# Kernel tuning notes

Measured on AMD Instinct MI355X. Metric: run time of the kernel, lower is better.

The kernel has to match this reference:

```python
import jax, jax.numpy as jnp
import numpy as np

N, D, K = 131072, 64, 512
COMMITMENT_COST = 0.25
DECAY = 0.99
EPSILON = 1e-05


def setup_inputs() -> dict:
    key = jax.random.key(0)
    k1, k2, k3 = jax.random.split(key, 3)
    return {
        "inputs": jax.random.normal(k1, (N, D), dtype=jnp.float32),
        "embedding_weight": jax.random.normal(k2, (K, D), dtype=jnp.float32),
        "ema_w": jax.random.normal(k3, (K, D), dtype=jnp.float32),
        "ema_cluster_size": jnp.zeros((K,), dtype=jnp.float32),
    }


def reference(inputs, embedding_weight, ema_w, ema_cluster_size):
    num_embeddings = embedding_weight.shape[0]
    distances = (
        jnp.sum(inputs ** 2, axis=1, keepdims=True)
        + jnp.sum(embedding_weight ** 2, axis=1)
        - 2.0 * jnp.matmul(inputs, embedding_weight.T)
    )
    encoding_indices = jnp.argmin(distances, axis=1)  # [N]
    # dense one-hot (returned by the module); float32 instead of torch double
    encodings = jax.nn.one_hot(encoding_indices, num_embeddings, dtype=jnp.float32)
    # encodings @ W is just a codebook gather
    quantized = jnp.take(embedding_weight, encoding_indices, axis=0)  # [N, D]

    # ---- EMA codebook update (training path; all detached from autodiff) ----
    counts = jax.ops.segment_sum(
        jnp.ones((inputs.shape[0],), dtype=jnp.float32),
        encoding_indices, num_segments=num_embeddings)  # == encodings.sum(0)
    new_cluster_size = ema_cluster_size * DECAY + (1.0 - DECAY) * counts
    n = jnp.sum(new_cluster_size)
    new_cluster_size = (new_cluster_size + EPSILON) / (n + num_embeddings * EPSILON) * n
    # dw = encodings^T @ inputs -> scatter-add of inputs per code
    dw = jax.ops.segment_sum(inputs, encoding_indices, num_segments=num_embeddings)
    new_ema_w = ema_w * DECAY + (1.0 - DECAY) * dw
    new_embedding = new_ema_w / new_cluster_size[:, None]
    new_cluster_size = jax.lax.stop_gradient(new_cluster_size)
    new_ema_w = jax.lax.stop_gradient(new_ema_w)
    new_embedding = jax.lax.stop_gradient(new_embedding)

    # commitment loss (quantized detached)
    e_latent_loss = jnp.mean((jax.lax.stop_gradient(quantized) - inputs) ** 2)
    loss = COMMITMENT_COST * e_latent_loss
    # straight-through estimator
    quantized_st = inputs + jax.lax.stop_gradient(quantized - inputs)

    avg_probs = jnp.mean(encodings, axis=0)
    perplexity = jnp.exp(-jnp.sum(avg_probs * jnp.log(avg_probs + 1e-10)))
    return (loss, quantized_st, perplexity, encodings,
            new_embedding, new_cluster_size, new_ema_w)
```

## Files before the change

### kernel.cpp

```cpp
#include <hip/hip_runtime.h>

#define NROWS 131072
#define DDIM  64
#define KCODE 512

#define QUANT_OFF 1LL
#define PERP_OFF  8388609LL
#define ENC_OFF   8388610LL
#define EMB_OFF   75497474LL
#define CS_OFF    75530242LL
#define EMAW_OFF  75530754LL

#define WS_COUNTS 0
#define WS_NEGWN  512
#define WS_SSE    1024
#define WS_DW     1040
#define WS_ZERO_FLOATS 33808
#define WS_OFF    33808
#define WS_POS    34320
#define WS_IDX    34832
#define WS_BUCKET 165904
#define WS_WHI    296976
#define WS_WMID   313360
#define WS_WLO    329744

using short8 = __attribute__((ext_vector_type(8))) short;
using f32x4  = __attribute__((ext_vector_type(4))) float;

#define MFMA(a, b, c) __builtin_amdgcn_mfma_f32_16x16x32_bf16((a), (b), (c), 0, 0, 0)

__device__ inline unsigned short bf16_rne(float x) {
    unsigned u = __float_as_uint(x);
    unsigned r = u + 0x7FFFu + ((u >> 16) & 1u);
    return (unsigned short)(r >> 16);
}
__device__ inline float bf16_to_f(unsigned short h) {
    return __uint_as_float((unsigned)h << 16);
}
__device__ inline void split3(const float* v, short8& h8, short8& m8, short8& l8) {
#pragma unroll
    for (int j = 0; j < 8; ++j) {
        float x = v[j];
        unsigned short h = bf16_rne(x);
        float m_ = x - bf16_to_f(h);
        unsigned short m = bf16_rne(m_);
        float l_ = m_ - bf16_to_f(m);
        unsigned short l = bf16_rne(l_);
        h8[j] = (short)h; m8[j] = (short)m; l8[j] = (short)l;
    }
}

__global__ __launch_bounds__(256) void prep_kernel(
    const float* __restrict__ W, ushort* __restrict__ whi,
    ushort* __restrict__ wmid, ushort* __restrict__ wlo,
    float* __restrict__ negwn, float* __restrict__ enc) {
    if (blockIdx.x == 8) {
        if (threadIdx.x == 0) {
            enc[0] = 0.f; enc[1] = 0.f;
            enc[67108862ULL] = 0.f; enc[67108863ULL] = 0.f;
        }
        for (int k = threadIdx.x; k < KCODE; k += 256) {
            const float4* wr = reinterpret_cast<const float4*>(&W[(size_t)k * DDIM]);
            float s = 0.f;
#pragma unroll
            for (int i = 0; i < DDIM / 4; ++i) {
                float4 v = wr[i];
                s += v.x * v.x + v.y * v.y + v.z * v.z + v.w * v.w;
            }
            negwn[k] = -0.5f * s;
        }
        return;
    }
    int t = blockIdx.x * 256 + threadIdx.x;
    int lane = t & 63;
    int code = (t >> 6) * 16 + (lane & 15);
    int kbase = (lane >> 4) * 8;
    int obase = t * 16;
#pragma unroll
    for (int kh = 0; kh < 2; ++kh) {
        float xbuf[8];
#pragma unroll
        for (int j = 0; j < 8; ++j) xbuf[j] = W[code * 64 + kh * 32 + kbase + j];
        short8 h8, m8, l8;
        split3(xbuf, h8, m8, l8);
#pragma unroll
        for (int j = 0; j < 8; ++j) {
            whi[obase + kh * 8 + j]  = (ushort)h8[j];
            wmid[obase + kh * 8 + j] = (ushort)m8[j];
            wlo[obase + kh * 8 + j]  = (ushort)l8[j];
        }
    }
}

__global__ __launch_bounds__(256) void vq_main_kernel(
    const float* __restrict__ X, const ushort* __restrict__ WHI,
    const ushort* __restrict__ WMID, const ushort* __restrict__ WLO,
    const float* __restrict__ negwn, const float* __restrict__ W,
    float* __restrict__ counts, float* __restrict__ sse_g,
    int* __restrict__ idx_out, float* __restrict__ outq) {

    __shared__ int rowIdx[128];
    const int tid = threadIdx.x;
    const int wave = tid >> 6, lane = tid & 63;
    const int col = lane & 15, kg = lane >> 4;
    const int row0 = blockIdx.x * 128;
    const int rowbase = row0 + wave * 32;

    short8 xh[2][2], xm[2][2], xl[2][2];
#pragma unroll
    for (int t = 0; t < 2; ++t) {
        int row = rowbase + t * 16 + col;
#pragma unroll
        for (int kh = 0; kh < 2; ++kh) {
            const float4* p = reinterpret_cast<const float4*>(&X[row * 64 + kh * 32 + kg * 8]);
            float4 a = p[0], b = p[1];
            float xbuf[8] = {a.x, a.y, a.z, a.w, b.x, b.y, b.z, b.w};
            split3(xbuf, xh[t][kh], xm[t][kh], xl[t][kh]);
        }
    }

    float bestV[2][4]; int bestC[2][4];
#pragma unroll
    for (int t = 0; t < 2; ++t)
#pragma unroll
        for (int i = 0; i < 4; ++i) { bestV[t][i] = -3.4e38f; bestC[t][i] = 0; }

    for (int c = 0; c < 32; ++c) {
        const short8* ph = reinterpret_cast<const short8*>(&WHI[(c * 64 + lane) * 16]);
        const short8* pm = reinterpret_cast<const short8*>(&WMID[(c * 64 + lane) * 16]);
        const short8* pl = reinterpret_cast<const short8*>(&WLO[(c * 64 + lane) * 16]);
        short8 wh0 = ph[0], wh1 = ph[1];
        short8 wm0 = pm[0], wm1 = pm[1];
        short8 wl0 = pl[0], wl1 = pl[1];
        float wn = negwn[c * 16 + col];
#pragma unroll
        for (int t = 0; t < 2; ++t) {
            f32x4 acc = {0.f, 0.f, 0.f, 0.f};
            acc = MFMA(xh[t][0], wl0, acc); acc = MFMA(xh[t][1], wl1, acc);
            acc = MFMA(xl[t][0], wh0, acc); acc = MFMA(xl[t][1], wh1, acc);
            acc = MFMA(xm[t][0], wm0, acc); acc = MFMA(xm[t][1], wm1, acc);
            acc = MFMA(xh[t][0], wm0, acc); acc = MFMA(xh[t][1], wm1, acc);
            acc = MFMA(xm[t][0], wh0, acc); acc = MFMA(xm[t][1], wh1, acc);
            acc = MFMA(xh[t][0], wh0, acc); acc = MFMA(xh[t][1], wh1, acc);
#pragma unroll
            for (int i = 0; i < 4; ++i) {
                float r = acc[i] + wn;
                if (r > bestV[t][i]) { bestV[t][i] = r; bestC[t][i] = c; }
            }
        }
    }

#pragma unroll
    for (int t = 0; t < 2; ++t)
#pragma unroll
        for (int i = 0; i < 4; ++i) {
            float v = bestV[t][i];
            int ix = bestC[t][i] * 16 + col;
#pragma unroll
            for (int m = 1; m <= 8; m <<= 1) {
                float ov = __shfl_xor(v, m);
                int   oi = __shfl_xor(ix, m);
                if (ov > v || (ov == v && oi < ix)) { v = ov; ix = oi; }
            }
            if (col == 0) rowIdx[wave * 32 + t * 16 + kg * 4 + i] = ix;
        }
    __syncthreads();

    float ssel = 0.f;
    for (int u = tid; u < 128 * 16; u += 256) {
        int r = u >> 4, d4 = (u & 15) << 2;
        int ix = rowIdx[r];
        float4 wv = *reinterpret_cast<const float4*>(&W[ix * 64 + d4]);
        float4 xv = *reinterpret_cast<const float4*>(&X[(size_t)(row0 + r) * 64 + d4]);
        float dx = wv.x - xv.x, dy = wv.y - xv.y, dz = wv.z - xv.z, dw4 = wv.w - xv.w;
        ssel += dx * dx + dy * dy + dz * dz + dw4 * dw4;
        size_t ob = (size_t)(row0 + r) * 64 + d4;
        outq[ob + 0] = xv.x + dx;
        outq[ob + 1] = xv.y + dy;
        outq[ob + 2] = xv.z + dz;
        outq[ob + 3] = xv.w + dw4;
    }
#pragma unroll
    for (int m = 32; m >= 1; m >>= 1) ssel += __shfl_xor(ssel, m);
    if (lane == 0) atomicAdd(sse_g, ssel);

    if (tid < 128) {
        int ix = rowIdx[tid];
        idx_out[row0 + tid] = ix;
        atomicAdd(&counts[ix], 1.0f);
    }
}

__global__ void enc_ones_kernel(const int* __restrict__ idx, float* __restrict__ enc) {
    int i = blockIdx.x * 256 + threadIdx.x;
    enc[(size_t)i * KCODE + idx[i]] = 1.0f;
}

__global__ void prefix_kernel(const float* __restrict__ counts,
                              int* __restrict__ off, int* __restrict__ pos) {
    __shared__ int tmp[512];
    int t = threadIdx.x;
    int c = (int)counts[t];
    tmp[t] = c;
    __syncthreads();
    int val = c;
    for (int s = 1; s < 512; s <<= 1) {
        int add = (t >= s) ? tmp[t - s] : 0;
        __syncthreads();
        val += add; tmp[t] = val;
        __syncthreads();
    }
    int excl = val - c;
    off[t] = excl; pos[t] = excl;
}

__global__ void scatter_kernel(const int* __restrict__ idx, int* __restrict__ pos,
                               int* __restrict__ bucket) {
    int i = blockIdx.x * 256 + threadIdx.x;
    int k = idx[i];
    int p = atomicAdd(&pos[k], 1);
    bucket[p] = (k << 17) | i;
}

__global__ __launch_bounds__(256) void dwsum_kernel(
    const float* __restrict__ X, const int* __restrict__ bucket,
    float* __restrict__ dw) {
    const int lane = threadIdx.x & 63;
    const int gwave = (blockIdx.x * 256 + threadIdx.x) >> 6;
    const int r0 = gwave * 16;
    int v = bucket[r0];
    int k = v >> 17, row = v & 0x1FFFF;
    float acc = 0.f;
#pragma unroll
    for (int i = 0; i < 16; ++i) {
        acc += X[(size_t)row * 64 + lane];
        if (i + 1 < 16) {
            int nv = bucket[r0 + i + 1];
            int nk = nv >> 17, nrow = nv & 0x1FFFF;
            if (nk != k) {
                atomicAdd(&dw[k * 64 + lane], acc);
                acc = 0.f; k = nk;
            }
            row = nrow;
        }
    }
    atomicAdd(&dw[k * 64 + lane], acc);
}

__global__ __launch_bounds__(512) void finalize_kernel(
    const float* __restrict__ ema_w, const float* __restrict__ ema_cs,
    const float* __restrict__ counts, const float* __restrict__ dw,
    const float* __restrict__ sse_g, float* __restrict__ out) {

    __shared__ float red[512];
    __shared__ float cs_sh[512];
    int t = threadIdx.x;

    float cnt = counts[t];
    float raw = ema_cs[t] * 0.99f + 0.01f * cnt;
    red[t] = raw;
    __syncthreads();
    for (int s = 256; s > 0; s >>= 1) {
        if (t < s) red[t] += red[t + s];
        __syncthreads();
    }
    float n = red[0];
    __syncthreads();

    float ncs = (raw + 1e-5f) / (n + (float)KCODE * 1e-5f) * n;
    out[CS_OFF + t] = ncs;
    cs_sh[t] = ncs;

    float avg = cnt / (float)NROWS;
    red[t] = avg * logf(avg + 1e-10f);
    __syncthreads();
    for (int s = 256; s > 0; s >>= 1) {
        if (t < s) red[t] += red[t + s];
        __syncthreads();
    }
    if (t == 0) {
        out[PERP_OFF] = expf(-red[0]);
        out[0] = 0.25f * sse_g[0] / ((float)NROWS * (float)DDIM);
    }
    __syncthreads();

    for (int i = t; i < KCODE * DDIM; i += 512) {
        float ne = ema_w[i] * 0.99f + 0.01f * dw[i];
        out[EMAW_OFF + i] = ne;
        out[EMB_OFF + i] = ne / cs_sh[i >> 6];
    }
}

extern "C" void kernel_launch(void* const* d_in, const int* in_sizes, int n_in,
                              void* d_out, int out_size, void* d_ws, size_t ws_size,
                              hipStream_t stream) {
    const float* X      = (const float*)d_in[0];
    const float* W      = (const float*)d_in[1];
    const float* ema_w  = (const float*)d_in[2];
    const float* ema_cs = (const float*)d_in[3];
    float* out = (float*)d_out;
    float* ws  = (float*)d_ws;

    float*  counts = ws + WS_COUNTS;
    float*  negwn  = ws + WS_NEGWN;
    float*  sse    = ws + WS_SSE;
    float*  dw     = ws + WS_DW;
    int*    off    = (int*)(ws + WS_OFF);
    int*    pos    = (int*)(ws + WS_POS);
    int*    idx    = (int*)(ws + WS_IDX);
    int*    bucket = (int*)(ws + WS_BUCKET);
    ushort* whi    = (ushort*)(ws + WS_WHI);
    ushort* wmid   = (ushort*)(ws + WS_WMID);
    ushort* wlo    = (ushort*)(ws + WS_WLO);

    float* enc = out + ENC_OFF;

    (void)hipMemsetAsync(d_ws, 0, (size_t)WS_ZERO_FLOATS * sizeof(float), stream);
    (void)hipMemsetAsync(enc + 2, 0, 268435440ULL, stream);

    prep_kernel<<<9, 256, 0, stream>>>(W, whi, wmid, wlo, negwn, enc);
    vq_main_kernel<<<NROWS / 128, 256, 0, stream>>>(X, whi, wmid, wlo, negwn, W,
                                                    counts, sse, idx,
                                                    out + QUANT_OFF);
    enc_ones_kernel<<<NROWS / 256, 256, 0, stream>>>(idx, out + ENC_OFF);
    prefix_kernel<<<1, 512, 0, stream>>>(counts, off, pos);
    scatter_kernel<<<NROWS / 256, 256, 0, stream>>>(idx, pos, bucket);
    dwsum_kernel<<<NROWS / 16 / 4, 256, 0, stream>>>(X, bucket, dw);
    finalize_kernel<<<1, 512, 0, stream>>>(ema_w, ema_cs, counts, dw, sse, out);
}
```

Before: 296.0 us.

## Fuse one-hot zeroing and ones writes into the main VQ kernel

The separate memset of the dense one-hot encodings buffer and the enc_ones kernel are removed. Instead, each thread of the main distance/argmin kernel zeroes half of one row of the encodings with nontemporal 8-byte stores, spread across the codebook loop. After the argmin it writes the 1.0 for that row. The aim is to overlap the large zero-fill with MFMA compute and to drop a kernel launch plus an index re-read. The cost is extra store traffic inside the compute loop, which may compete with the codebook loads.

```diff
diff --git a/kernel.cpp b/kernel.cpp
--- a/kernel.cpp
+++ b/kernel.cpp
@@ -26,6 +26,7 @@
 
 using short8 = __attribute__((ext_vector_type(8))) short;
 using f32x4  = __attribute__((ext_vector_type(4))) float;
+using f32x2  = __attribute__((ext_vector_type(2))) float;
 
 #define MFMA(a, b, c) __builtin_amdgcn_mfma_f32_16x16x32_bf16((a), (b), (c), 0, 0, 0)
 
@@ -53,12 +54,8 @@
 __global__ __launch_bounds__(256) void prep_kernel(
     const float* __restrict__ W, ushort* __restrict__ whi,
     ushort* __restrict__ wmid, ushort* __restrict__ wlo,
-    float* __restrict__ negwn, float* __restrict__ enc) {
+    float* __restrict__ negwn) {
     if (blockIdx.x == 8) {
-        if (threadIdx.x == 0) {
-            enc[0] = 0.f; enc[1] = 0.f;
-            enc[67108862ULL] = 0.f; enc[67108863ULL] = 0.f;
-        }
         for (int k = threadIdx.x; k < KCODE; k += 256) {
             const float4* wr = reinterpret_cast<const float4*>(&W[(size_t)k * DDIM]);
             float s = 0.f;
@@ -97,7 +94,8 @@
     const ushort* __restrict__ WMID, const ushort* __restrict__ WLO,
     const float* __restrict__ negwn, const float* __restrict__ W,
     float* __restrict__ counts, float* __restrict__ sse_g,
-    int* __restrict__ idx_out, float* __restrict__ outq) {
+    int* __restrict__ idx_out, float* __restrict__ outq,
+    float* __restrict__ enc) {
 
     __shared__ int rowIdx[128];
     const int tid = threadIdx.x;
@@ -106,6 +104,9 @@
     const int row0 = blockIdx.x * 128;
     const int rowbase = row0 + wave * 32;
 
+    float* zp = enc + ((size_t)(row0 + (tid >> 1)) << 9) + ((tid & 1) << 8);
+    const f32x2 zz = {0.f, 0.f};
+
     short8 xh[2][2], xm[2][2], xl[2][2];
 #pragma unroll
     for (int t = 0; t < 2; ++t) {
@@ -126,6 +127,10 @@
         for (int i = 0; i < 4; ++i) { bestV[t][i] = -3.4e38f; bestC[t][i] = 0; }
 
     for (int c = 0; c < 32; ++c) {
+#pragma unroll
+        for (int j = 0; j < 4; ++j)
+            __builtin_nontemporal_store(zz, reinterpret_cast<f32x2*>(zp + c * 8 + j * 2));
+
         const short8* ph = reinterpret_cast<const short8*>(&WHI[(c * 64 + lane) * 16]);
         const short8* pm = reinterpret_cast<const short8*>(&WMID[(c * 64 + lane) * 16]);
         const short8* pl = reinterpret_cast<const short8*>(&WLO[(c * 64 + lane) * 16]);
@@ -165,6 +170,13 @@
             if (col == 0) rowIdx[wave * 32 + t * 16 + kg * 4 + i] = ix;
         }
     __syncthreads();
+
+    {
+        int r = tid >> 1, h = tid & 1;
+        int ix = rowIdx[r];
+        if ((ix >> 8) == h)
+            enc[((size_t)(row0 + r) << 9) + ix] = 1.0f;
+    }
 
     float ssel = 0.f;
     for (int u = tid; u < 128 * 16; u += 256) {
@@ -191,11 +203,6 @@
     }
 }
 
-__global__ void enc_ones_kernel(const int* __restrict__ idx, float* __restrict__ enc) {
-    int i = blockIdx.x * 256 + threadIdx.x;
-    enc[(size_t)i * KCODE + idx[i]] = 1.0f;
-}
-
 __global__ void prefix_kernel(const float* __restrict__ counts,
                               int* __restrict__ off, int* __restrict__ pos) {
     __shared__ int tmp[512];
@@ -313,16 +320,12 @@
     ushort* wmid   = (ushort*)(ws + WS_WMID);
     ushort* wlo    = (ushort*)(ws + WS_WLO);
 
-    float* enc = out + ENC_OFF;
-
     (void)hipMemsetAsync(d_ws, 0, (size_t)WS_ZERO_FLOATS * sizeof(float), stream);
-    (void)hipMemsetAsync(enc + 2, 0, 268435440ULL, stream);
-
-    prep_kernel<<<9, 256, 0, stream>>>(W, whi, wmid, wlo, negwn, enc);
+
+    prep_kernel<<<9, 256, 0, stream>>>(W, whi, wmid, wlo, negwn);
     vq_main_kernel<<<NROWS / 128, 256, 0, stream>>>(X, whi, wmid, wlo, negwn, W,
                                                     counts, sse, idx,
-                                                    out + QUANT_OFF);
-    enc_ones_kernel<<<NROWS / 256, 256, 0, stream>>>(idx, out + ENC_OFF);
+                                                    out + QUANT_OFF, out + ENC_OFF);
     prefix_kernel<<<1, 512, 0, stream>>>(counts, off, pos);
     scatter_kernel<<<NROWS / 256, 256, 0, stream>>>(idx, pos, bucket);
     dwsum_kernel<<<NROWS / 16 / 4, 256, 0, stream>>>(X, bucket, dw);
```

After: 970.4 us. 3.28x slower.
